# Performance work log

Hardware: AMD Instinct MI355X
Metric: run time of the kernel (lower is better)

Reference implementation:

```python
import jax, jax.numpy as jnp
import numpy as np
from jax import lax

B, C, HID, H, W = 8, 256, 64, 64, 64

def conv3x3(x, w, b):
    # x: [B,C_in,H,W], w: [C_out,C_in,3,3], b: [C_out]
    y = lax.conv_general_dilated(x, w, window_strides=(1, 1), padding='SAME',
                                 dimension_numbers=('NCHW', 'OIHW', 'NCHW'))
    return y + b[None, :, None, None]

def setup_inputs() -> dict:
    key = jax.random.key(0)
    ks = jax.random.split(key, 7)
    s_in = 1.0 / np.sqrt(C * 9)
    return {
        'x': jax.random.normal(ks[0], (B, C, H, W), dtype=jnp.float32),
        'Wq': jax.random.normal(ks[1], (HID, C, 3, 3), dtype=jnp.float32) * s_in,
        'bq': jax.random.normal(ks[2], (HID,), dtype=jnp.float32) * s_in,
        'Wk': jax.random.normal(ks[3], (HID, C, 3, 3), dtype=jnp.float32) * s_in,
        'bk': jax.random.normal(ks[4], (HID,), dtype=jnp.float32) * s_in,
        'Wv': jax.random.normal(ks[5], (C, C, 3, 3), dtype=jnp.float32) * s_in,
        'bv': jax.random.normal(ks[6], (C,), dtype=jnp.float32) * s_in,
    }

def reference(x, Wq, bq, Wk, bk, Wv, bv):
    b, c, w, h = x.shape
    n = w * h
    q = conv3x3(x, Wq, bq).reshape(b, -1, n).transpose(0, 2, 1)  # [B,N,hid]
    k = conv3x3(x, Wk, bk).reshape(b, -1, n)                      # [B,hid,N]
    v = conv3x3(x, Wv, bv).reshape(b, c, n)                       # [B,C,N]
    attn = jax.nn.softmax(jnp.einsum('bnd,bdm->bnm', q, k), axis=-1)  # [B,N,N]
    # out = bmm(value, attn^T): out[b,c,m] = sum_n v[b,c,n] * attn[b,m,n]
    out = jnp.einsum('bcn,bmn->bcm', v, attn).reshape(b, c, w, h)
    # F.interpolate(out, h, mode='bilinear') with H==W is an exact identity
    return out + x
```

## Files before the change

### kernel.cpp

```cpp
#include <hip/hip_runtime.h>
#include <math.h>

#define NB   8
#define NC   256
#define ND   64
#define NPIX 4096
#define LSTR 72

typedef short bf16x8 __attribute__((ext_vector_type(8)));
typedef float f32x4  __attribute__((ext_vector_type(4)));
typedef float f32x16 __attribute__((ext_vector_type(16)));

static __device__ __forceinline__ ushort f2bf(float f) {
    uint u = __float_as_uint(f);
    u += 0x7fffu + ((u >> 16) & 1u);
    return (ushort)(u >> 16);
}
static __device__ __forceinline__ float bf2f(ushort h) {
    return __uint_as_float(((uint)h) << 16);
}

__global__ __launch_bounds__(256) void transpose_x(
    const float* __restrict__ x, ushort* __restrict__ xth, ushort* __restrict__ xtl)
{
    __shared__ float tile[64][68];
    const int t = threadIdx.x;
    const int p0 = blockIdx.x * 64, c0 = blockIdx.y * 64, b = blockIdx.z;

    const int cl = t >> 4, p4 = (t & 15) * 4;
    #pragma unroll
    for (int i = 0; i < 4; i++) {
        const int c = cl + 16 * i;
        *(float4*)&tile[c][p4] =
            *(const float4*)&x[((size_t)(b * NC + c0 + c)) * NPIX + p0 + p4];
    }
    __syncthreads();

    const int pl = t & 63, ch = t >> 6;
    float v[16];
    #pragma unroll
    for (int j = 0; j < 16; j++) v[j] = tile[ch * 16 + j][pl];
    ushort h[16], l[16];
    #pragma unroll
    for (int j = 0; j < 16; j++) {
        h[j] = f2bf(v[j]);
        l[j] = f2bf(v[j] - bf2f(h[j]));
    }
    const size_t o = ((size_t)(b * NPIX + p0 + pl)) * 256 + c0 + ch * 16;
    *(uint4*)&xth[o]     = *(uint4*)&h[0];
    *(uint4*)&xth[o + 8] = *(uint4*)&h[8];
    *(uint4*)&xtl[o]     = *(uint4*)&l[0];
    *(uint4*)&xtl[o + 8] = *(uint4*)&l[8];
}

__global__ __launch_bounds__(256) void transpose_w(
    const float* __restrict__ Wq, const float* __restrict__ Wk,
    const float* __restrict__ Wv,
    ushort* __restrict__ qh, ushort* __restrict__ ql,
    ushort* __restrict__ kh, ushort* __restrict__ kl,
    ushort* __restrict__ vh)
{
    __shared__ float wb[2304];
    const int g = blockIdx.x, t = threadIdx.x;
    const float* src;
    ushort *dh, *dl;
    int co, Co, split;
    if (g < 64)       { src = Wq + (size_t)g * 2304; co = g;       Co = 64;  dh = qh; dl = ql; split = 1; }
    else if (g < 128) { src = Wk + (size_t)(g - 64) * 2304; co = g - 64; Co = 64; dh = kh; dl = kl; split = 1; }
    else              { src = Wv + (size_t)(g - 128) * 2304; co = g - 128; Co = 256; dh = vh; dl = nullptr; split = 0; }

    for (int i = t; i < 2304; i += 256) wb[i] = src[i];
    __syncthreads();
    for (int j = t; j < 2304; j += 256) {
        const int rs = j >> 8, ci = j & 255;
        const float v = wb[ci * 9 + rs];
        const ushort hv = f2bf(v);
        const size_t o = ((size_t)(rs * Co + co)) * 256 + ci;
        dh[o] = hv;
        if (split) dl[o] = f2bf(v - bf2f(hv));
    }
}

__global__ __launch_bounds__(256) void conv_split_k(
    const ushort* __restrict__ xth, const ushort* __restrict__ xtl,
    const ushort* __restrict__ wqh, const ushort* __restrict__ wql,
    const ushort* __restrict__ wkh, const ushort* __restrict__ wkl,
    const float* __restrict__ bq, const float* __restrict__ bk,
    ushort* __restrict__ qoh, ushort* __restrict__ qol,
    ushort* __restrict__ koh, ushort* __restrict__ kol)
{
    extern __shared__ char smem[];
    ushort* xsh = (ushort*)smem;
    ushort* xsl = xsh + 6 * 66 * 24;
    ushort* wsp = xsl + 6 * 66 * 24;
    float*  sbias = (float*)(wsp + 9 * 64 * 24);

    const int hq = blockIdx.x, b = blockIdx.y, ct = blockIdx.z;
    const ushort* wth = ct ? wkh : wqh;
    const ushort* wtl = ct ? wkl : wql;
    const float*  bias = ct ? bk : bq;
    ushort* outh = ct ? koh : qoh;
    ushort* outl = ct ? kol : qol;

    const int t = threadIdx.x;
    const int wv = t >> 6, lane = t & 63;
    const int l31 = lane & 31, khl = lane >> 5;
    const int lanebase = l31 * 24 + khl * 8;
    const int h = hq * 4 + wv;

    if (t < 64) sbias[t] = bias[t];
    for (int i = t; i < 384; i += 256) {
        const int p = i / 192, r2 = i % 192;
        const int row = r2 / 32, e = (r2 % 32) / 16, ci = r2 & 15;
        (p ? xsl : xsh)[(row * 66 + e * 65) * 24 + ci] = 0;
    }

    f32x16 a00 = {0}, a01 = {0}, a10 = {0}, a11 = {0};

    for (int ch = 0; ch < 16; ch++) {
        __syncthreads();
        const int ci0 = ch * 16;
        #pragma unroll
        for (int pl2 = 0; pl2 < 2; pl2++) {
            const ushort* src = pl2 ? xtl : xth;
            ushort* dst = pl2 ? xsl : xsh;
            #pragma unroll
            for (int i = 0; i < 3; i++) {
                const int a = i * 256 + t;
                const int cih = a & 1, col = (a >> 1) & 63, row = a >> 7;
                const int hs = hq * 4 + row - 1;
                uint4 val = {0, 0, 0, 0};
                if (hs >= 0 && hs < 64)
                    val = *(const uint4*)&src[((size_t)(b * NPIX + hs * 64 + col)) * 256 + ci0 + cih * 8];
                *(uint4*)&dst[(row * 66 + 1 + col) * 24 + cih * 8] = val;
            }
        }
        #pragma unroll
        for (int i = 0; i < 5; i++) {
            const int a = i * 256 + t;
            if (a < 1152) {
                const int cih = a & 1, co = (a >> 1) & 63, rs = a >> 7;
                uint4 wv4 = *(const uint4*)&wth[((size_t)(rs * 64 + co)) * 256 + ci0 + cih * 8];
                *(uint4*)&wsp[(rs * 64 + co) * 24 + cih * 8] = wv4;
            }
        }
        __syncthreads();
        #pragma unroll
        for (int rs = 0; rs < 9; rs++) {
            const int r = rs / 3, s = rs % 3;
            bf16x8 A0 = *(const bf16x8*)&wsp[rs * 1536 + lanebase];
            bf16x8 A1 = *(const bf16x8*)&wsp[rs * 1536 + 768 + lanebase];
            const int xo = ((wv + r) * 66 + s) * 24 + lanebase;
            bf16x8 B0h = *(const bf16x8*)&xsh[xo];
            bf16x8 B1h = *(const bf16x8*)&xsh[xo + 768];
            bf16x8 B0l = *(const bf16x8*)&xsl[xo];
            bf16x8 B1l = *(const bf16x8*)&xsl[xo + 768];
            a00 = __builtin_amdgcn_mfma_f32_32x32x16_bf16(A0, B0h, a00, 0, 0, 0);
            a01 = __builtin_amdgcn_mfma_f32_32x32x16_bf16(A0, B1h, a01, 0, 0, 0);
            a10 = __builtin_amdgcn_mfma_f32_32x32x16_bf16(A1, B0h, a10, 0, 0, 0);
            a11 = __builtin_amdgcn_mfma_f32_32x32x16_bf16(A1, B1h, a11, 0, 0, 0);
            a00 = __builtin_amdgcn_mfma_f32_32x32x16_bf16(A0, B0l, a00, 0, 0, 0);
            a01 = __builtin_amdgcn_mfma_f32_32x32x16_bf16(A0, B1l, a01, 0, 0, 0);
            a10 = __builtin_amdgcn_mfma_f32_32x32x16_bf16(A1, B0l, a10, 0, 0, 0);
            a11 = __builtin_amdgcn_mfma_f32_32x32x16_bf16(A1, B1l, a11, 0, 0, 0);
        }
        __syncthreads();
        #pragma unroll
        for (int i = 0; i < 5; i++) {
            const int a = i * 256 + t;
            if (a < 1152) {
                const int cih = a & 1, co = (a >> 1) & 63, rs = a >> 7;
                uint4 wv4 = *(const uint4*)&wtl[((size_t)(rs * 64 + co)) * 256 + ci0 + cih * 8];
                *(uint4*)&wsp[(rs * 64 + co) * 24 + cih * 8] = wv4;
            }
        }
        __syncthreads();
        #pragma unroll
        for (int rs = 0; rs < 9; rs++) {
            const int r = rs / 3, s = rs % 3;
            bf16x8 A0 = *(const bf16x8*)&wsp[rs * 1536 + lanebase];
            bf16x8 A1 = *(const bf16x8*)&wsp[rs * 1536 + 768 + lanebase];
            const int xo = ((wv + r) * 66 + s) * 24 + lanebase;
            bf16x8 B0h = *(const bf16x8*)&xsh[xo];
            bf16x8 B1h = *(const bf16x8*)&xsh[xo + 768];
            a00 = __builtin_amdgcn_mfma_f32_32x32x16_bf16(A0, B0h, a00, 0, 0, 0);
            a01 = __builtin_amdgcn_mfma_f32_32x32x16_bf16(A0, B1h, a01, 0, 0, 0);
            a10 = __builtin_amdgcn_mfma_f32_32x32x16_bf16(A1, B0h, a10, 0, 0, 0);
            a11 = __builtin_amdgcn_mfma_f32_32x32x16_bf16(A1, B1h, a11, 0, 0, 0);
        }
    }

    const float4* sb4 = (const float4*)sbias;
    #pragma unroll
    for (int ms = 0; ms < 2; ms++)
        #pragma unroll
        for (int ns = 0; ns < 2; ns++) {
            const f32x16 av = ms ? (ns ? a11 : a10) : (ns ? a01 : a00);
            const int p = h * 64 + ns * 32 + l31;
            #pragma unroll
            for (int g = 0; g < 4; g++) {
                const float4 bi = sb4[ms * 8 + 2 * g + khl];
                float v0 = av[4 * g + 0] + bi.x;
                float v1 = av[4 * g + 1] + bi.y;
                float v2 = av[4 * g + 2] + bi.z;
                float v3 = av[4 * g + 3] + bi.w;
                ushort4 hv, lv;
                hv.x = f2bf(v0); lv.x = f2bf(v0 - bf2f(hv.x));
                hv.y = f2bf(v1); lv.y = f2bf(v1 - bf2f(hv.y));
                hv.z = f2bf(v2); lv.z = f2bf(v2 - bf2f(hv.z));
                hv.w = f2bf(v3); lv.w = f2bf(v3 - bf2f(hv.w));
                const size_t o = ((size_t)(b * NPIX + p)) * 64 + ms * 32 + 8 * g + 4 * khl;
                *(ushort4*)&outh[o] = hv;
                *(ushort4*)&outl[o] = lv;
            }
        }
}

__global__ __launch_bounds__(256) void conv_v_k(
    const ushort* __restrict__ xth, const ushort* __restrict__ wtv,
    const float* __restrict__ bv, ushort* __restrict__ vout)
{
    extern __shared__ char smem[];
    ushort* xsh = (ushort*)smem;
    ushort* wsp = xsh + 6 * 66 * 24;
    float*  sbias = (float*)(wsp + 9 * 64 * 24);

    const int hq = blockIdx.x, b = blockIdx.y, co0 = blockIdx.z * 64;
    const int t = threadIdx.x;
    const int wv = t >> 6, lane = t & 63;
    const int l31 = lane & 31, khl = lane >> 5;
    const int lanebase = l31 * 24 + khl * 8;
    const int h = hq * 4 + wv;

    if (t < 64) sbias[t] = bv[co0 + t];
    for (int i = t; i < 192; i += 256) {
        const int row = i / 32, e = (i % 32) / 16, ci = i & 15;
        xsh[(row * 66 + e * 65) * 24 + ci] = 0;
    }

    f32x16 a00 = {0}, a01 = {0}, a10 = {0}, a11 = {0};

    for (int ch = 0; ch < 16; ch++) {
        __syncthreads();
        const int ci0 = ch * 16;
        #pragma unroll
        for (int i = 0; i < 3; i++) {
            const int a = i * 256 + t;
            const int cih = a & 1, col = (a >> 1) & 63, row = a >> 7;
            const int hs = hq * 4 + row - 1;
            uint4 val = {0, 0, 0, 0};
            if (hs >= 0 && hs < 64)
                val = *(const uint4*)&xth[((size_t)(b * NPIX + hs * 64 + col)) * 256 + ci0 + cih * 8];
            *(uint4*)&xsh[(row * 66 + 1 + col) * 24 + cih * 8] = val;
        }
        #pragma unroll
        for (int i = 0; i < 5; i++) {
            const int a = i * 256 + t;
            if (a < 1152) {
                const int cih = a & 1, co = (a >> 1) & 63, rs = a >> 7;
                uint4 wv4 = *(const uint4*)&wtv[((size_t)(rs * 256 + co0 + co)) * 256 + ci0 + cih * 8];
                *(uint4*)&wsp[(rs * 64 + co) * 24 + cih * 8] = wv4;
            }
        }
        __syncthreads();
        #pragma unroll
        for (int rs = 0; rs < 9; rs++) {
            const int r = rs / 3, s = rs % 3;
            const int xo = ((wv + r) * 66 + s) * 24 + lanebase;
            bf16x8 A0 = *(const bf16x8*)&xsh[xo];
            bf16x8 A1 = *(const bf16x8*)&xsh[xo + 768];
            bf16x8 B0 = *(const bf16x8*)&wsp[rs * 1536 + lanebase];
            bf16x8 B1 = *(const bf16x8*)&wsp[rs * 1536 + 768 + lanebase];
            a00 = __builtin_amdgcn_mfma_f32_32x32x16_bf16(A0, B0, a00, 0, 0, 0);
            a01 = __builtin_amdgcn_mfma_f32_32x32x16_bf16(A0, B1, a01, 0, 0, 0);
            a10 = __builtin_amdgcn_mfma_f32_32x32x16_bf16(A1, B0, a10, 0, 0, 0);
            a11 = __builtin_amdgcn_mfma_f32_32x32x16_bf16(A1, B1, a11, 0, 0, 0);
        }
    }

    #pragma unroll
    for (int ns = 0; ns < 2; ns++) {
        const int co = co0 + ns * 32 + l31;
        const float bi = sbias[ns * 32 + l31];
        #pragma unroll
        for (int ms = 0; ms < 2; ms++) {
            const f32x16 av = ms ? (ns ? a11 : a10) : (ns ? a01 : a00);
            #pragma unroll
            for (int g = 0; g < 4; g++) {
                const int p = h * 64 + ms * 32 + 8 * g + 4 * khl;
                ushort4 ov;
                ov.x = f2bf(av[4 * g + 0] + bi);
                ov.y = f2bf(av[4 * g + 1] + bi);
                ov.z = f2bf(av[4 * g + 2] + bi);
                ov.w = f2bf(av[4 * g + 3] + bi);
                *(ushort4*)&vout[((size_t)(b * NC + co)) * NPIX + p] = ov;
            }
        }
    }
}

__global__ __launch_bounds__(256, 2) void attn_k(
    const ushort* __restrict__ qh, const ushort* __restrict__ ql,
    const ushort* __restrict__ kh, const ushort* __restrict__ kl,
    const ushort* __restrict__ vb, const float* __restrict__ x,
    float* __restrict__ out)
{
    const int b    = blockIdx.y;
    const int m0   = blockIdx.x * 64;
    const int t    = threadIdx.x;
    const int wave = t >> 6;
    const int lane = t & 63;
    const int quad = lane >> 4;
    const int l16  = lane & 15;

    __shared__ __align__(16) char smem[65792];
    ushort* sqh = (ushort*)(smem);
    ushort* sql = (ushort*)(smem + 9216);
    ushort* skh = (ushort*)(smem + 18432);
    ushort* skl = (ushort*)(smem + 27648);
    ushort* svs = (ushort*)(smem + 18432);
    ushort* sps = (ushort*)(smem + 55296);
    float*  red = (float*)(smem + 64512);
    float*  ivl = (float*)(smem + 65536);

    {
        const int r = t >> 2, dc = (t & 3) * 16;
        const size_t g = ((size_t)b * NPIX + m0 + r) * ND + dc;
        uint4 a0 = *(const uint4*)&qh[g];
        uint4 a1 = *(const uint4*)&qh[g + 8];
        *(uint4*)&sqh[r * LSTR + dc]     = a0;
        *(uint4*)&sqh[r * LSTR + dc + 8] = a1;
        uint4 b0 = *(const uint4*)&ql[g];
        uint4 b1 = *(const uint4*)&ql[g + 8];
        *(uint4*)&sql[r * LSTR + dc]     = b0;
        *(uint4*)&sql[r * LSTR + dc + 8] = b1;
    }

    f32x4 acc[16];
    #pragma unroll
    for (int i = 0; i < 16; i++) acc[i] = (f32x4){0.f, 0.f, 0.f, 0.f};
    float rsum = 0.f;
    const int rs_row = t & 63, rs_c = (t >> 6) * 16;

    for (int n0 = 0; n0 < NPIX; n0 += 64) {
        __syncthreads();
        {
            const int r = t >> 2, dc = (t & 3) * 16;
            const size_t g = ((size_t)b * NPIX + n0 + r) * ND + dc;
            uint4 a0 = *(const uint4*)&kh[g];
            uint4 a1 = *(const uint4*)&kh[g + 8];
            *(uint4*)&skh[r * LSTR + dc]     = a0;
            *(uint4*)&skh[r * LSTR + dc + 8] = a1;
            uint4 b0 = *(const uint4*)&kl[g];
            uint4 b1 = *(const uint4*)&kl[g + 8];
            *(uint4*)&skl[r * LSTR + dc]     = b0;
            *(uint4*)&skl[r * LSTR + dc + 8] = b1;
        }
        __syncthreads();

        bf16x8 aqh[2], aql[2];
        const int am = 16 * wave + l16;
        #pragma unroll
        for (int ks = 0; ks < 2; ks++) {
            aqh[ks] = *(const bf16x8*)&sqh[am * LSTR + ks * 32 + quad * 8];
            aql[ks] = *(const bf16x8*)&sql[am * LSTR + ks * 32 + quad * 8];
        }
        #pragma unroll
        for (int nt = 0; nt < 4; nt++) {
            f32x4 s = {0.f, 0.f, 0.f, 0.f};
            const int bn = nt * 16 + l16;
            #pragma unroll
            for (int ks = 0; ks < 2; ks++) {
                bf16x8 bh = *(const bf16x8*)&skh[bn * LSTR + ks * 32 + quad * 8];
                bf16x8 bl = *(const bf16x8*)&skl[bn * LSTR + ks * 32 + quad * 8];
                s = __builtin_amdgcn_mfma_f32_16x16x32_bf16(aqh[ks], bh, s, 0, 0, 0);
                s = __builtin_amdgcn_mfma_f32_16x16x32_bf16(aql[ks], bh, s, 0, 0, 0);
                s = __builtin_amdgcn_mfma_f32_16x16x32_bf16(aqh[ks], bl, s, 0, 0, 0);
            }
            #pragma unroll
            for (int r = 0; r < 4; r++) {
                float p = __expf(s[r] - 30.f);
                sps[(16 * wave + quad * 4 + r) * LSTR + nt * 16 + l16] = f2bf(p);
            }
        }
        __syncthreads();

        {
            const int c0 = t >> 2, ncs = (t & 3) * 16;
            #pragma unroll
            for (int cc = 0; cc < 4; cc++) {
                const int c = cc * 64 + c0;
                const size_t g = ((size_t)b * NC + c) * NPIX + n0 + ncs;
                uint4 a0 = *(const uint4*)&vb[g];
                uint4 a1 = *(const uint4*)&vb[g + 8];
                *(uint4*)&svs[c * LSTR + ncs]     = a0;
                *(uint4*)&svs[c * LSTR + ncs + 8] = a1;
            }
            uint4 p0 = *(const uint4*)&sps[rs_row * LSTR + rs_c];
            uint4 p1 = *(const uint4*)&sps[rs_row * LSTR + rs_c + 8];
            const ushort* pu0 = (const ushort*)&p0;
            const ushort* pu1 = (const ushort*)&p1;
            float ss = 0.f;
            #pragma unroll
            for (int i = 0; i < 8; i++) ss += bf2f(pu0[i]) + bf2f(pu1[i]);
            rsum += ss;
        }
        __syncthreads();

        bf16x8 ap[4][2];
        #pragma unroll
        for (int ms = 0; ms < 4; ms++)
            #pragma unroll
            for (int ks = 0; ks < 2; ks++)
                ap[ms][ks] = *(const bf16x8*)&sps[(16 * ms + l16) * LSTR + ks * 32 + quad * 8];
        #pragma unroll
        for (int ct = 0; ct < 4; ct++) {
            const int c = 64 * wave + ct * 16 + l16;
            #pragma unroll
            for (int ks = 0; ks < 2; ks++) {
                bf16x8 bv = *(const bf16x8*)&svs[c * LSTR + ks * 32 + quad * 8];
                #pragma unroll
                for (int ms = 0; ms < 4; ms++)
                    acc[ms * 4 + ct] = __builtin_amdgcn_mfma_f32_16x16x32_bf16(
                        ap[ms][ks], bv, acc[ms * 4 + ct], 0, 0, 0);
            }
        }
    }

    red[(t & 63) * 4 + (t >> 6)] = rsum;
    __syncthreads();
    if (t < 64)
        ivl[t] = 1.f / (red[t * 4 + 0] + red[t * 4 + 1] + red[t * 4 + 2] + red[t * 4 + 3]);
    __syncthreads();

    #pragma unroll
    for (int ms = 0; ms < 4; ms++) {
        const float il0 = ivl[16 * ms + quad * 4 + 0];
        const float il1 = ivl[16 * ms + quad * 4 + 1];
        const float il2 = ivl[16 * ms + quad * 4 + 2];
        const float il3 = ivl[16 * ms + quad * 4 + 3];
        const int m = m0 + 16 * ms + quad * 4;
        #pragma unroll
        for (int ct = 0; ct < 4; ct++) {
            const int c = 64 * wave + ct * 16 + l16;
            const size_t base = ((size_t)b * NC + c) * NPIX + m;
            float4 xv = *(const float4*)&x[base];
            f32x4 a = acc[ms * 4 + ct];
            float4 o;
            o.x = fmaf(a[0], il0, xv.x);
            o.y = fmaf(a[1], il1, xv.y);
            o.z = fmaf(a[2], il2, xv.z);
            o.w = fmaf(a[3], il3, xv.w);
            *(float4*)&out[base] = o;
        }
    }
}

extern "C" void kernel_launch(void* const* d_in, const int* in_sizes, int n_in,
                              void* d_out, int out_size, void* d_ws, size_t ws_size,
                              hipStream_t stream)
{
    const float* x  = (const float*)d_in[0];
    const float* Wq = (const float*)d_in[1];
    const float* bq = (const float*)d_in[2];
    const float* Wk = (const float*)d_in[3];
    const float* bk = (const float*)d_in[4];
    const float* Wv = (const float*)d_in[5];
    const float* bv = (const float*)d_in[6];
    float* outp = (float*)d_out;

    const size_t XT = (size_t)NB * NPIX * 256;
    const size_t QK = (size_t)NB * NPIX * ND;
    ushort* xt_h = (ushort*)d_ws;
    ushort* xt_l = xt_h + XT;
    ushort* v_b  = xt_l;
    ushort* q_h  = xt_l + XT;
    ushort* q_l  = q_h + QK;
    ushort* k_h  = q_l + QK;
    ushort* k_l  = k_h + QK;
    ushort* wtq_h = k_l + QK;
    ushort* wtq_l = wtq_h + 147456;
    ushort* wtk_h = wtq_l + 147456;
    ushort* wtk_l = wtk_h + 147456;
    ushort* wtv_h = wtk_l + 147456;

    dim3 blk(256);
    transpose_x<<<dim3(64, 4, NB), blk, 0, stream>>>(x, xt_h, xt_l);
    transpose_w<<<dim3(384), blk, 0, stream>>>(Wq, Wk, Wv, wtq_h, wtq_l, wtk_h, wtk_l, wtv_h);
    conv_split_k<<<dim3(16, NB, 2), blk, 65920, stream>>>(
        xt_h, xt_l, wtq_h, wtq_l, wtk_h, wtk_l, bq, bk, q_h, q_l, k_h, k_l);
    conv_v_k<<<dim3(16, NB, 4), blk, 46912, stream>>>(xt_h, wtv_h, bv, v_b);
    attn_k<<<dim3(64, NB), blk, 0, stream>>>(q_h, q_l, k_h, k_l, v_b, x, outp);
}
```

Before: 427.8 us.

## Keep Q/K/V fragments in registers and double-buffer P to cut attention syncs

The attention kernel now loads Q fragments into registers once and streams K and V fragments straight from global memory into registers, prefetching the next tile while the current one computes. K and V no longer pass through shared memory. P is written to a double-buffered LDS tile, so each iteration needs only one barrier instead of three. Row sums are kept per lane and reduced with shuffles, and the grid is flattened so batch varies fastest. The aim is to remove LDS staging traffic and barrier stalls, at the cost of higher register pressure and uncoalesced, fragment-shaped global loads for K and V.

New measurement: 425.1 us. Within noise of the previous version (-0.6%).

```diff
diff --git a/kernel.cpp b/kernel.cpp
--- a/kernel.cpp
+++ b/kernel.cpp
@@ -305,152 +305,143 @@
     const ushort* __restrict__ vb, const float* __restrict__ x,
     float* __restrict__ out)
 {
-    const int b    = blockIdx.y;
-    const int m0   = blockIdx.x * 64;
-    const int t    = threadIdx.x;
-    const int wave = t >> 6;
+    const int id = blockIdx.x;
+    const int b  = id & 7;
+    const int m0 = (id >> 3) * 64;
+    const int t  = threadIdx.x;
+    const int w  = t >> 6;
     const int lane = t & 63;
     const int quad = lane >> 4;
     const int l16  = lane & 15;
 
-    __shared__ __align__(16) char smem[65792];
-    ushort* sqh = (ushort*)(smem);
-    ushort* sql = (ushort*)(smem + 9216);
-    ushort* skh = (ushort*)(smem + 18432);
-    ushort* skl = (ushort*)(smem + 27648);
-    ushort* svs = (ushort*)(smem + 18432);
-    ushort* sps = (ushort*)(smem + 55296);
-    float*  red = (float*)(smem + 64512);
-    float*  ivl = (float*)(smem + 65536);
-
-    {
-        const int r = t >> 2, dc = (t & 3) * 16;
-        const size_t g = ((size_t)b * NPIX + m0 + r) * ND + dc;
-        uint4 a0 = *(const uint4*)&qh[g];
-        uint4 a1 = *(const uint4*)&qh[g + 8];
-        *(uint4*)&sqh[r * LSTR + dc]     = a0;
-        *(uint4*)&sqh[r * LSTR + dc + 8] = a1;
-        uint4 b0 = *(const uint4*)&ql[g];
-        uint4 b1 = *(const uint4*)&ql[g + 8];
-        *(uint4*)&sql[r * LSTR + dc]     = b0;
-        *(uint4*)&sql[r * LSTR + dc + 8] = b1;
-    }
-
-    f32x4 acc[16];
-    #pragma unroll
-    for (int i = 0; i < 16; i++) acc[i] = (f32x4){0.f, 0.f, 0.f, 0.f};
-    float rsum = 0.f;
-    const int rs_row = t & 63, rs_c = (t >> 6) * 16;
+    __shared__ ushort sps[2][64 * LSTR];
+    __shared__ float  red[4][64];
+    __shared__ float  ivl[64];
+
+    bf16x8 aqh[4][2], aql[4][2];
+    #pragma unroll
+    for (int mg = 0; mg < 4; mg++)
+        #pragma unroll
+        for (int ks = 0; ks < 2; ks++) {
+            const size_t g = ((size_t)b * NPIX + m0 + mg * 16 + l16) * ND + ks * 32 + quad * 8;
+            aqh[mg][ks] = *(const bf16x8*)&qh[g];
+            aql[mg][ks] = *(const bf16x8*)&ql[g];
+        }
+
+    const size_t kbase = ((size_t)b * NPIX + 16 * w + l16) * ND + quad * 8;
+    size_t vbase[4];
+    #pragma unroll
+    for (int ct = 0; ct < 4; ct++)
+        vbase[ct] = ((size_t)b * NC + 64 * w + ct * 16 + l16) * NPIX + quad * 8;
+
+    bf16x8 kfh[2], kfl[2], vf[4][2];
+    #pragma unroll
+    for (int ks = 0; ks < 2; ks++) {
+        kfh[ks] = *(const bf16x8*)&kh[kbase + ks * 32];
+        kfl[ks] = *(const bf16x8*)&kl[kbase + ks * 32];
+    }
+    #pragma unroll
+    for (int ct = 0; ct < 4; ct++)
+        #pragma unroll
+        for (int ks = 0; ks < 2; ks++)
+            vf[ct][ks] = *(const bf16x8*)&vb[vbase[ct] + ks * 32];
+
+    f32x4 acc[4][4];
+    #pragma unroll
+    for (int i = 0; i < 4; i++)
+        #pragma unroll
+        for (int j = 0; j < 4; j++) acc[i][j] = (f32x4){0.f, 0.f, 0.f, 0.f};
+    float lsum[4] = {0.f, 0.f, 0.f, 0.f};
 
     for (int n0 = 0; n0 < NPIX; n0 += 64) {
-        __syncthreads();
-        {
-            const int r = t >> 2, dc = (t & 3) * 16;
-            const size_t g = ((size_t)b * NPIX + n0 + r) * ND + dc;
-            uint4 a0 = *(const uint4*)&kh[g];
-            uint4 a1 = *(const uint4*)&kh[g + 8];
-            *(uint4*)&skh[r * LSTR + dc]     = a0;
-            *(uint4*)&skh[r * LSTR + dc + 8] = a1;
-            uint4 b0 = *(const uint4*)&kl[g];
-            uint4 b1 = *(const uint4*)&kl[g + 8];
-            *(uint4*)&skl[r * LSTR + dc]     = b0;
-            *(uint4*)&skl[r * LSTR + dc + 8] = b1;
-        }
-        __syncthreads();
-
-        bf16x8 aqh[2], aql[2];
-        const int am = 16 * wave + l16;
+        const int buf = (n0 >> 6) & 1;
+        const bool nxt = (n0 + 64) < NPIX;
+
+        #pragma unroll
+        for (int mg = 0; mg < 4; mg++) {
+            f32x4 s = {0.f, 0.f, 0.f, 0.f};
+            #pragma unroll
+            for (int ks = 0; ks < 2; ks++) {
+                s = __builtin_amdgcn_mfma_f32_16x16x32_bf16(kfh[ks], aqh[mg][ks], s, 0, 0, 0);
+                s = __builtin_amdgcn_mfma_f32_16x16x32_bf16(kfl[ks], aqh[mg][ks], s, 0, 0, 0);
+                s = __builtin_amdgcn_mfma_f32_16x16x32_bf16(kfh[ks], aql[mg][ks], s, 0, 0, 0);
+            }
+            uint2 pk;
+            {
+                const ushort p0 = f2bf(__expf(s[0] - 30.f));
+                const ushort p1 = f2bf(__expf(s[1] - 30.f));
+                const ushort p2 = f2bf(__expf(s[2] - 30.f));
+                const ushort p3 = f2bf(__expf(s[3] - 30.f));
+                lsum[mg] += (bf2f(p0) + bf2f(p1)) + (bf2f(p2) + bf2f(p3));
+                pk.x = (uint)p0 | ((uint)p1 << 16);
+                pk.y = (uint)p2 | ((uint)p3 << 16);
+            }
+            *(uint2*)&sps[buf][(mg * 16 + l16) * LSTR + 16 * w + quad * 4] = pk;
+        }
+
+        if (nxt) {
+            const size_t kb = kbase + (size_t)(n0 + 64) * ND;
+            #pragma unroll
+            for (int ks = 0; ks < 2; ks++) {
+                kfh[ks] = *(const bf16x8*)&kh[kb + ks * 32];
+                kfl[ks] = *(const bf16x8*)&kl[kb + ks * 32];
+            }
+        }
+        __syncthreads();
+
         #pragma unroll
         for (int ks = 0; ks < 2; ks++) {
-            aqh[ks] = *(const bf16x8*)&sqh[am * LSTR + ks * 32 + quad * 8];
-            aql[ks] = *(const bf16x8*)&sql[am * LSTR + ks * 32 + quad * 8];
-        }
-        #pragma unroll
-        for (int nt = 0; nt < 4; nt++) {
-            f32x4 s = {0.f, 0.f, 0.f, 0.f};
-            const int bn = nt * 16 + l16;
-            #pragma unroll
-            for (int ks = 0; ks < 2; ks++) {
-                bf16x8 bh = *(const bf16x8*)&skh[bn * LSTR + ks * 32 + quad * 8];
-                bf16x8 bl = *(const bf16x8*)&skl[bn * LSTR + ks * 32 + quad * 8];
-                s = __builtin_amdgcn_mfma_f32_16x16x32_bf16(aqh[ks], bh, s, 0, 0, 0);
-                s = __builtin_amdgcn_mfma_f32_16x16x32_bf16(aql[ks], bh, s, 0, 0, 0);
-                s = __builtin_amdgcn_mfma_f32_16x16x32_bf16(aqh[ks], bl, s, 0, 0, 0);
-            }
-            #pragma unroll
-            for (int r = 0; r < 4; r++) {
-                float p = __expf(s[r] - 30.f);
-                sps[(16 * wave + quad * 4 + r) * LSTR + nt * 16 + l16] = f2bf(p);
-            }
-        }
-        __syncthreads();
-
-        {
-            const int c0 = t >> 2, ncs = (t & 3) * 16;
-            #pragma unroll
-            for (int cc = 0; cc < 4; cc++) {
-                const int c = cc * 64 + c0;
-                const size_t g = ((size_t)b * NC + c) * NPIX + n0 + ncs;
-                uint4 a0 = *(const uint4*)&vb[g];
-                uint4 a1 = *(const uint4*)&vb[g + 8];
-                *(uint4*)&svs[c * LSTR + ncs]     = a0;
-                *(uint4*)&svs[c * LSTR + ncs + 8] = a1;
-            }
-            uint4 p0 = *(const uint4*)&sps[rs_row * LSTR + rs_c];
-            uint4 p1 = *(const uint4*)&sps[rs_row * LSTR + rs_c + 8];
-            const ushort* pu0 = (const ushort*)&p0;
-            const ushort* pu1 = (const ushort*)&p1;
-            float ss = 0.f;
-            #pragma unroll
-            for (int i = 0; i < 8; i++) ss += bf2f(pu0[i]) + bf2f(pu1[i]);
-            rsum += ss;
-        }
-        __syncthreads();
-
-        bf16x8 ap[4][2];
-        #pragma unroll
-        for (int ms = 0; ms < 4; ms++)
-            #pragma unroll
-            for (int ks = 0; ks < 2; ks++)
-                ap[ms][ks] = *(const bf16x8*)&sps[(16 * ms + l16) * LSTR + ks * 32 + quad * 8];
-        #pragma unroll
-        for (int ct = 0; ct < 4; ct++) {
-            const int c = 64 * wave + ct * 16 + l16;
-            #pragma unroll
-            for (int ks = 0; ks < 2; ks++) {
-                bf16x8 bv = *(const bf16x8*)&svs[c * LSTR + ks * 32 + quad * 8];
+            bf16x8 ap[4];
+            #pragma unroll
+            for (int mg = 0; mg < 4; mg++)
+                ap[mg] = *(const bf16x8*)&sps[buf][(mg * 16 + l16) * LSTR + ks * 32 + quad * 8];
+            #pragma unroll
+            for (int mg = 0; mg < 4; mg++)
                 #pragma unroll
-                for (int ms = 0; ms < 4; ms++)
-                    acc[ms * 4 + ct] = __builtin_amdgcn_mfma_f32_16x16x32_bf16(
-                        ap[ms][ks], bv, acc[ms * 4 + ct], 0, 0, 0);
-            }
-        }
-    }
-
-    red[(t & 63) * 4 + (t >> 6)] = rsum;
+                for (int ct = 0; ct < 4; ct++)
+                    acc[mg][ct] = __builtin_amdgcn_mfma_f32_16x16x32_bf16(
+                        ap[mg], vf[ct][ks], acc[mg][ct], 0, 0, 0);
+        }
+
+        if (nxt) {
+            #pragma unroll
+            for (int ct = 0; ct < 4; ct++)
+                #pragma unroll
+                for (int ks = 0; ks < 2; ks++)
+                    vf[ct][ks] = *(const bf16x8*)&vb[vbase[ct] + n0 + 64 + ks * 32];
+        }
+    }
+
+    #pragma unroll
+    for (int mg = 0; mg < 4; mg++) {
+        lsum[mg] += __shfl_xor(lsum[mg], 16, 64);
+        lsum[mg] += __shfl_xor(lsum[mg], 32, 64);
+    }
+    if (quad == 0) {
+        #pragma unroll
+        for (int mg = 0; mg < 4; mg++) red[w][mg * 16 + l16] = lsum[mg];
+    }
     __syncthreads();
     if (t < 64)
-        ivl[t] = 1.f / (red[t * 4 + 0] + red[t * 4 + 1] + red[t * 4 + 2] + red[t * 4 + 3]);
+        ivl[t] = 1.f / (red[0][t] + red[1][t] + red[2][t] + red[3][t]);
     __syncthreads();
 
     #pragma unroll
-    for (int ms = 0; ms < 4; ms++) {
-        const float il0 = ivl[16 * ms + quad * 4 + 0];
-        const float il1 = ivl[16 * ms + quad * 4 + 1];
-        const float il2 = ivl[16 * ms + quad * 4 + 2];
-        const float il3 = ivl[16 * ms + quad * 4 + 3];
-        const int m = m0 + 16 * ms + quad * 4;
+    for (int mg = 0; mg < 4; mg++) {
+        const int mrow = mg * 16 + quad * 4;
+        const float4 il4 = *(const float4*)&ivl[mrow];
+        const int m = m0 + mrow;
         #pragma unroll
         for (int ct = 0; ct < 4; ct++) {
-            const int c = 64 * wave + ct * 16 + l16;
+            const int c = 64 * w + ct * 16 + l16;
             const size_t base = ((size_t)b * NC + c) * NPIX + m;
-            float4 xv = *(const float4*)&x[base];
-            f32x4 a = acc[ms * 4 + ct];
+            const float4 xv = *(const float4*)&x[base];
+            const f32x4 a = acc[mg][ct];
             float4 o;
-            o.x = fmaf(a[0], il0, xv.x);
-            o.y = fmaf(a[1], il1, xv.y);
-            o.z = fmaf(a[2], il2, xv.z);
-            o.w = fmaf(a[3], il3, xv.w);
+            o.x = fmaf(a[0], il4.x, xv.x);
+            o.y = fmaf(a[1], il4.y, xv.y);
+            o.z = fmaf(a[2], il4.z, xv.z);
+            o.w = fmaf(a[3], il4.w, xv.w);
             *(float4*)&out[base] = o;
         }
     }
@@ -490,5 +481,5 @@
     conv_split_k<<<dim3(16, NB, 2), blk, 65920, stream>>>(
         xt_h, xt_l, wtq_h, wtq_l, wtk_h, wtk_l, bq, bk, q_h, q_l, k_h, k_l);
     conv_v_k<<<dim3(16, NB, 4), blk, 46912, stream>>>(xt_h, wtv_h, bv, v_b);
-    attn_k<<<dim3(64, NB), blk, 0, stream>>>(q_h, q_l, k_h, k_l, v_b, x, outp);
-}
+    attn_k<<<dim3(512), blk, 0, stream>>>(q_h, q_l, k_h, k_l, v_b, x, outp);
+}
```
